# Performance work log

Measured on AMD Instinct MI355X. Metric: run time of the kernel, lower is better.

## Reference

```python
import jax, jax.numpy as jnp
from jax import lax
import numpy as np

# Layer configuration (from init_kwargs; see FilteringActLayer.__init__)
UP = 2                      # up_factor (temp_rate 32 / in_rate 16)
DOWN = 2                    # down_factor (temp_rate 32 / out_rate 16)
PADDING = (11, 10, 11, 10)  # (px0, px1, py0, py1), derived pad_total = 21
GAIN = float(np.sqrt(2.0))  # lrelu gain used in StyleGAN3
SLOPE = 0.2                 # leaky relu negative slope
CLAMP = 256.0               # activation clamp
UP_TAPS = 12
IN_CUTOFF = 8.0
OUT_CUTOFF = 8.0
IN_HALF_WIDTH = 6.0
OUT_HALF_WIDTH = 6.0
TEMP_FS = 32.0              # max(in_rate, out_rate) * act_upsampling


def _design_lowpass(numtaps, cutoff, width, fs):
    """Replicates scipy.signal.firwin(numtaps, cutoff, width=width, fs=fs)."""
    nyq = fs / 2.0
    # kaiser_atten / kaiser_beta
    atten = 2.285 * (numtaps - 1) * np.pi * (width / nyq) + 7.95
    if atten > 50.0:
        beta = 0.1102 * (atten - 8.7)
    elif atten > 21.0:
        beta = 0.5842 * (atten - 21.0) ** 0.4 + 0.07886 * (atten - 21.0)
    else:
        beta = 0.0
    m = np.arange(numtaps) - (numtaps - 1) / 2.0
    c = cutoff / nyq
    h = c * np.sinc(c * m)
    h = h * np.kaiser(numtaps, beta)
    h = h / np.sum(h)  # unity gain at DC (firwin scale=True)
    return h.astype(np.float32)


def _upfirdn2d_sep(x, f, up, down, pad, gain):
    """Zero-insert upsample by `up`, pad, correlate with separable 1D FIR f
    (applied flipped, i.e. true convolution as in the torch reference),
    then subsample by `down`. x: [N,C,H,W], f: [taps]."""
    N, C, H, W = x.shape
    fr = f[::-1].astype(x.dtype)
    kH = fr.reshape(1, 1, -1, 1)
    kW = fr.reshape(1, 1, 1, -1)
    px0, px1, py0, py1 = pad
    xr = x.reshape(N * C, 1, H, W)
    # lhs_dilation implements the zero-insertion; +up-1 hi-pad accounts for the
    # trailing zeros the torch reference keeps after upsampling.
    xr = lax.conv_general_dilated(xr, kH, window_strides=(down, 1),
                                  padding=((py0, py1 + up - 1), (0, 0)),
                                  lhs_dilation=(up, 1))
    xr = lax.conv_general_dilated(xr, kW, window_strides=(1, down),
                                  padding=((0, 0), (px0, px1 + up - 1)),
                                  lhs_dilation=(1, up))
    Ho, Wo = xr.shape[2], xr.shape[3]
    return xr.reshape(N, C, Ho, Wo) * gain


def setup_inputs() -> dict:
    key = jax.random.key(0)
    k1, k2 = jax.random.split(key)
    x = jax.random.normal(k1, (8, 512, 64, 64), dtype=jnp.float32)
    bias = jax.random.normal(k2, (512,), dtype=jnp.float32) * 0.1
    up_filter = jnp.asarray(_design_lowpass(UP_TAPS, IN_CUTOFF, IN_HALF_WIDTH * 2, TEMP_FS))
    down_filter = jnp.asarray(_design_lowpass(UP_TAPS, OUT_CUTOFF, OUT_HALF_WIDTH * 2, TEMP_FS))
    return {"x": x, "bias": bias, "up_filter": up_filter, "down_filter": down_filter}


def reference(x, bias, up_filter, down_filter):
    # (1) FIR upsample (gain = up^2 to preserve signal magnitude)
    y = _upfirdn2d_sep(x, up_filter, UP, 1, PADDING, float(UP * UP))
    # (2) bias + leaky-relu + gain + clamp (bias_act 'lrelu')
    y = y + bias[None, :, None, None]
    y = jnp.where(y >= 0, y, y * SLOPE) * GAIN
    y = jnp.clip(y, -CLAMP, CLAMP)
    # (3) FIR downsample
    y = _upfirdn2d_sep(y, down_filter, 1, DOWN, (0, 0, 0, 0), 1.0)
    return y
```

## Files before the change

### kernel.cpp

```cpp
#include <hip/hip_runtime.h>

#define SIN 80
#define ST1 80
#define ST3 72

typedef float v2f __attribute__((ext_vector_type(2)));

static __device__ __forceinline__ v2f fma2(v2f a, v2f b, v2f c) {
    return __builtin_elementwise_fma(a, b, c);
}
static __device__ __forceinline__ v2f bcast2(float s) {
    v2f r; r.x = s; r.y = s; return r;
}
static __device__ __forceinline__ v2f mk2(float a, float b) {
    v2f r; r.x = a; r.y = b; return r;
}

__global__ __launch_bounds__(256, 4)
void synth_fused(const float* __restrict__ x, const float* __restrict__ bias,
                 const float* __restrict__ fu, const float* __restrict__ fd,
                 float* __restrict__ out)
{
    __shared__ __align__(16) float bufA[3024];
    __shared__ __align__(16) float bufB[3376];
    __shared__ float sfilt[24];
    float* const s_in = bufA;
    float* const s_t3 = bufA;
    float* const s_t1 = bufB;

    const int tid  = threadIdx.x;
    const int bx   = blockIdx.x;
    const int tile = bx & 3;
    const int nc   = bx >> 2;
    const int gy0  = tile << 4;

    if (tid < 24) sfilt[tid] = (tid < 12) ? fu[tid] : fd[tid - 12];
    const float bc = bias[nc & 511];
    const float* __restrict__ xc = x + ((size_t)nc << 12);

    #pragma unroll
    for (int it = 0; it < 2; ++it) {
        int idx = tid + it * 256;
        if (idx < 416) {
            int r  = idx >> 4;
            int c4 = (idx & 15) << 2;
            int gy = gy0 - 5 + r;
            float4 v = make_float4(0.f, 0.f, 0.f, 0.f);
            if ((unsigned)gy < 64u)
                v = *reinterpret_cast<const float4*>(xc + (gy << 6) + c4);
            float* dst = s_in + r * SIN + 5 + c4;
            dst[0] = v.x; dst[1] = v.y; dst[2] = v.z; dst[3] = v.w;
        }
    }
    #pragma unroll
    for (int it = 0; it < 2; ++it) {
        int idx = tid + it * 256;
        if (idx < 416) {
            int r  = idx >> 4;
            int pc = idx & 15;
            int c  = (pc < 5) ? pc : (64 + pc);
            s_in[r * SIN + c] = 0.0f;
        }
    }
    __syncthreads();

    v2f upk[6], gpk[6];
    #pragma unroll
    for (int j = 0; j < 6; ++j) {
        upk[j] = mk2(sfilt[10 - 2*j], sfilt[11 - 2*j]);
        gpk[j] = mk2(sfilt[23 - 2*j], sfilt[22 - 2*j]);
    }

    if (tid < 222) {
        const int g3 = tid / 74;
        const int c  = tid - 74 * g3;
        const float* ip = s_in + (7 * g3) * SIN + c;
        float rv[12];
        #pragma unroll
        for (int j = 0; j < 12; ++j) rv[j] = ip[j * SIN];
        float* op = s_t1 + (14 * g3) * ST1 + c;
        #pragma unroll
        for (int m = 0; m < 7; ++m) {
            v2f acc = upk[0] * bcast2(rv[m]);
            #pragma unroll
            for (int j = 1; j < 6; ++j)
                acc = fma2(upk[j], bcast2(rv[m + j]), acc);
            op[(2*m) * ST1]     = acc.x;
            op[(2*m + 1) * ST1] = acc.y;
        }
    }
    __syncthreads();

    const float S42 = 4.0f * 1.41421356237309515f;
    v2f upk2[6];
    #pragma unroll
    for (int j = 0; j < 6; ++j) upk2[j] = upk[j] * S42;
    const float bcs = bc * 1.41421356237309515f;

    if (tid < 252) {
        const int r = tid / 6;
        const int q = tid - 6 * r;
        const float* t1r = s_t1 + r * ST1 + 12 * q;
        float w[22];
        #pragma unroll
        for (int j = 0; j < 11; ++j) {
            v2f v2 = *reinterpret_cast<const v2f*>(t1r + 2 * j);
            w[2*j] = v2.x; w[2*j+1] = v2.y;
        }
        const v2f bc2 = bcast2(bcs);
        v2f t2p[17];
        #pragma unroll
        for (int i = 0; i < 17; ++i) {
            v2f acc = bc2;
            #pragma unroll
            for (int j = 0; j < 6; ++j)
                acc = fma2(upk2[j], bcast2(w[i + j]), acc);
            v2f mx = __builtin_elementwise_max(acc, acc * 0.2f);
            t2p[i] = mk2(__builtin_amdgcn_fmed3f(mx.x, -256.0f, 256.0f),
                         __builtin_amdgcn_fmed3f(mx.y, -256.0f, 256.0f));
        }
        float* t3r = s_t3 + r * ST3 + 12 * q;
        #pragma unroll
        for (int i = 0; i < 3; ++i) {
            float4 o4;
            float* op = &o4.x;
            #pragma unroll
            for (int s = 0; s < 4; ++s) {
                const int oi = 4 * i + s;
                v2f acc = gpk[0] * t2p[oi];
                #pragma unroll
                for (int j = 1; j < 6; ++j) acc = fma2(gpk[j], t2p[oi + j], acc);
                op[s] = acc.x + acc.y;
            }
            *reinterpret_cast<float4*>(t3r + 4 * i) = o4;
        }
    }
    __syncthreads();

    {
        const int c  = tid & 63;
        const int rc = tid >> 6;
        const float* t3c = s_t3 + (rc << 3) * ST3 + c;
        v2f vp[9];
        #pragma unroll
        for (int m = 0; m < 9; ++m)
            vp[m] = mk2(t3c[(2*m) * ST3], t3c[(2*m + 1) * ST3]);
        float* op = out + ((size_t)nc << 12) + ((size_t)(gy0 + (rc << 2)) << 6) + c;
        #pragma unroll
        for (int i = 0; i < 4; ++i) {
            v2f acc = gpk[0] * vp[i];
            #pragma unroll
            for (int j = 1; j < 6; ++j) acc = fma2(gpk[j], vp[i + j], acc);
            op[(size_t)(i << 6)] = acc.x + acc.y;
        }
    }
}

extern "C" void kernel_launch(void* const* d_in, const int* in_sizes, int n_in,
                              void* d_out, int out_size, void* d_ws, size_t ws_size,
                              hipStream_t stream) {
    const float* x    = (const float*)d_in[0];
    const float* bias = (const float*)d_in[1];
    const float* fu   = (const float*)d_in[2];
    const float* fd   = (const float*)d_in[3];
    float* out        = (float*)d_out;

    dim3 grid(8 * 512 * 4);
    dim3 block(256);
    hipLaunchKernelGGL(synth_fused, grid, block, 0, stream, x, bias, fu, fd, out);
}
```

Baseline: 151.4 us.

## Double tile height to 32 rows with 512-thread blocks to cut halo overhead

Each block now processes a 32-row output tile using 512 threads instead of a 16-row tile with 256 threads, halving the grid. This cuts the relative halo recomputation and reload (input rows, vertical upsample rows) per output. The vertical upsample work split is reorganized into six groups, with the first group handling an extra row pair. The cost is more shared memory per block (about 45KB) and a stricter launch bound, which may lower occupancy.

After: 153.0 us. No clear change (+1.0%).

```diff
diff --git a/kernel.cpp b/kernel.cpp
--- a/kernel.cpp
+++ b/kernel.cpp
@@ -16,13 +16,13 @@
     v2f r; r.x = a; r.y = b; return r;
 }
 
-__global__ __launch_bounds__(256, 4)
+__global__ __launch_bounds__(512, 6)
 void synth_fused(const float* __restrict__ x, const float* __restrict__ bias,
                  const float* __restrict__ fu, const float* __restrict__ fd,
                  float* __restrict__ out)
 {
-    __shared__ __align__(16) float bufA[3024];
-    __shared__ __align__(16) float bufB[3376];
+    __shared__ __align__(16) float bufA[5328];
+    __shared__ __align__(16) float bufB[5928];
     __shared__ float sfilt[24];
     float* const s_in = bufA;
     float* const s_t3 = bufA;
@@ -30,9 +30,9 @@
 
     const int tid  = threadIdx.x;
     const int bx   = blockIdx.x;
-    const int tile = bx & 3;
-    const int nc   = bx >> 2;
-    const int gy0  = tile << 4;
+    const int tile = bx & 1;
+    const int nc   = bx >> 1;
+    const int gy0  = tile << 5;
 
     if (tid < 24) sfilt[tid] = (tid < 12) ? fu[tid] : fd[tid - 12];
     const float bc = bias[nc & 511];
@@ -40,8 +40,8 @@
 
     #pragma unroll
     for (int it = 0; it < 2; ++it) {
-        int idx = tid + it * 256;
-        if (idx < 416) {
+        int idx = tid + (it << 9);
+        if (idx < 672) {
             int r  = idx >> 4;
             int c4 = (idx & 15) << 2;
             int gy = gy0 - 5 + r;
@@ -54,8 +54,8 @@
     }
     #pragma unroll
     for (int it = 0; it < 2; ++it) {
-        int idx = tid + it * 256;
-        if (idx < 416) {
+        int idx = tid + (it << 9);
+        if (idx < 672) {
             int r  = idx >> 4;
             int pc = idx & 15;
             int c  = (pc < 5) ? pc : (64 + pc);
@@ -71,22 +71,32 @@
         gpk[j] = mk2(sfilt[23 - 2*j], sfilt[22 - 2*j]);
     }
 
-    if (tid < 222) {
-        const int g3 = tid / 74;
-        const int c  = tid - 74 * g3;
-        const float* ip = s_in + (7 * g3) * SIN + c;
+    if (tid < 444) {
+        const int g  = tid / 74;
+        const int c  = tid - 74 * g;
+        const int m0 = 6 * g + (g > 0);
+        const float* ip = s_in + m0 * SIN + c;
         float rv[12];
         #pragma unroll
-        for (int j = 0; j < 12; ++j) rv[j] = ip[j * SIN];
-        float* op = s_t1 + (14 * g3) * ST1 + c;
+        for (int j = 0; j < 11; ++j) rv[j] = ip[j * SIN];
+        rv[11] = (g == 0) ? ip[11 * SIN] : 0.0f;
+        float* op = s_t1 + (2 * m0) * ST1 + c;
         #pragma unroll
-        for (int m = 0; m < 7; ++m) {
-            v2f acc = upk[0] * bcast2(rv[m]);
+        for (int mm = 0; mm < 6; ++mm) {
+            v2f acc = upk[0] * bcast2(rv[mm]);
             #pragma unroll
             for (int j = 1; j < 6; ++j)
-                acc = fma2(upk[j], bcast2(rv[m + j]), acc);
-            op[(2*m) * ST1]     = acc.x;
-            op[(2*m + 1) * ST1] = acc.y;
+                acc = fma2(upk[j], bcast2(rv[mm + j]), acc);
+            op[(2*mm) * ST1]     = acc.x;
+            op[(2*mm + 1) * ST1] = acc.y;
+        }
+        if (g == 0) {
+            v2f acc = upk[0] * bcast2(rv[6]);
+            #pragma unroll
+            for (int j = 1; j < 6; ++j)
+                acc = fma2(upk[j], bcast2(rv[6 + j]), acc);
+            op[12 * ST1] = acc.x;
+            op[13 * ST1] = acc.y;
         }
     }
     __syncthreads();
@@ -97,7 +107,7 @@
     for (int j = 0; j < 6; ++j) upk2[j] = upk[j] * S42;
     const float bcs = bc * 1.41421356237309515f;
 
-    if (tid < 252) {
+    if (tid < 444) {
         const int r = tid / 6;
         const int q = tid - 6 * r;
         const float* t1r = s_t1 + r * ST1 + 12 * q;
@@ -165,7 +175,7 @@
     const float* fd   = (const float*)d_in[3];
     float* out        = (float*)d_out;
 
-    dim3 grid(8 * 512 * 4);
-    dim3 block(256);
+    dim3 grid(8 * 512 * 2);
+    dim3 block(512);
     hipLaunchKernelGGL(synth_fused, grid, block, 0, stream, x, bias, fu, fd, out);
 }
```
